# Optimization experiments

Measured on AMD Instinct MI355X. Metric: run time of the kernel, lower is better.

## Reference

```python
import jax, jax.numpy as jnp
import numpy as np

H = 2048
EPS = 1e-5  # torch LayerNorm default

def layer_norm(x, g, b):
    mu = jnp.mean(x, axis=-1, keepdims=True)
    var = jnp.mean(jnp.square(x - mu), axis=-1, keepdims=True)
    return (x - mu) * jax.lax.rsqrt(var + EPS) * g + b

def setup_inputs() -> dict:
    key = jax.random.key(0)
    ks = jax.random.split(key, 5)
    bound = 1.0 / np.sqrt(H)  # torch Linear default init range
    x = jax.random.normal(ks[0], (8192, H), dtype=jnp.float32)
    W1 = jax.random.uniform(ks[1], (H, H), jnp.float32, -bound, bound)
    b1 = jax.random.uniform(ks[2], (H,), jnp.float32, -bound, bound)
    W2 = jax.random.uniform(ks[3], (H, H), jnp.float32, -bound, bound)
    b2 = jax.random.uniform(ks[4], (H,), jnp.float32, -bound, bound)
    g1 = jnp.ones((H,), jnp.float32); be1 = jnp.zeros((H,), jnp.float32)
    g2 = jnp.ones((H,), jnp.float32); be2 = jnp.zeros((H,), jnp.float32)
    return {"x": x, "W1": W1, "b1": b1, "W2": W2, "b2": b2,
            "g1": g1, "be1": be1, "g2": g2, "be2": be2}

def reference(x, W1, b1, W2, b2, g1, be1, g2, be2):
    # ln1 -> linear1 -> relu -> (dropout p=0) -> ln2 -> linear2 -> (dropout p=0) -> +x -> relu
    out = layer_norm(x, g1, be1)
    out = jax.nn.relu(out @ W1.T + b1)
    out = layer_norm(out, g2, be2)
    out = out @ W2.T + b2
    return jax.nn.relu(out + x)
```

## Files before the change

### kernel.cpp

```cpp
#include <hip/hip_runtime.h>
#include <hip/hip_bf16.h>

#define H_DIM 2048
#define LN_EPS 1e-5f

typedef __bf16 bf16_t;
typedef __bf16 bf16x4 __attribute__((ext_vector_type(4)));
typedef __bf16 bf16x8 __attribute__((ext_vector_type(8)));
typedef float f32x4 __attribute__((ext_vector_type(4)));

__device__ __forceinline__ void async_copy16(const void* g, void* l) {
    __builtin_amdgcn_global_load_lds((const __attribute__((address_space(1))) void*)g,
                                     (__attribute__((address_space(3))) void*)l,
                                     16, 0, 0);
}

#define FENCE() asm volatile("" ::: "memory")
#define BARRIER() do { FENCE(); __builtin_amdgcn_s_barrier(); FENCE(); } while (0)

__global__ __launch_bounds__(256) void cast2_kernel(const float* __restrict__ w1,
                                                    const float* __restrict__ w2,
                                                    bf16_t* __restrict__ o1,
                                                    bf16_t* __restrict__ o2) {
    const int n4 = (H_DIM * H_DIM) / 4;
    int i = blockIdx.x * 256 + threadIdx.x;
    const float* src; bf16_t* dst; int j;
    if (i < n4) { src = w1; dst = o1; j = i; }
    else        { src = w2; dst = o2; j = i - n4; }
    float4 v = reinterpret_cast<const float4*>(src)[j];
    bf16x4 r;
    r[0] = (bf16_t)v.x; r[1] = (bf16_t)v.y; r[2] = (bf16_t)v.z; r[3] = (bf16_t)v.w;
    reinterpret_cast<bf16x4*>(dst)[j] = r;
}

__global__ __launch_bounds__(256) void ln_f32_v2(const float* __restrict__ in,
                                                 const float* __restrict__ g,
                                                 const float* __restrict__ b,
                                                 bf16_t* __restrict__ out,
                                                 bf16_t* __restrict__ xb) {
    const int l = threadIdx.x & 63, w = threadIdx.x >> 6;
    const size_t row = (size_t)blockIdx.x * 4 + w;
    const float* xr = in + row * H_DIM;
    float4 v[8];
    #pragma unroll
    for (int k = 0; k < 8; ++k) v[k] = reinterpret_cast<const float4*>(xr)[l + k * 64];
    float s = 0.f, s2 = 0.f;
    #pragma unroll
    for (int k = 0; k < 8; ++k) {
        s  += v[k].x + v[k].y + v[k].z + v[k].w;
        s2 += v[k].x * v[k].x + v[k].y * v[k].y + v[k].z * v[k].z + v[k].w * v[k].w;
    }
    #pragma unroll
    for (int off = 32; off > 0; off >>= 1) {
        s  += __shfl_down(s,  off, 64);
        s2 += __shfl_down(s2, off, 64);
    }
    s  = __shfl(s,  0, 64);
    s2 = __shfl(s2, 0, 64);
    float mu   = s * (1.f / H_DIM);
    float rstd = rsqrtf(s2 * (1.f / H_DIM) - mu * mu + LN_EPS);
    bf16_t* orow = out + row * H_DIM;
    bf16_t* xrow = xb ? xb + row * H_DIM : nullptr;
    #pragma unroll
    for (int k = 0; k < 8; ++k) {
        int c = l + k * 64;
        float4 gv = reinterpret_cast<const float4*>(g)[c];
        float4 bv = reinterpret_cast<const float4*>(b)[c];
        bf16x4 y;
        y[0] = (bf16_t)((v[k].x - mu) * rstd * gv.x + bv.x);
        y[1] = (bf16_t)((v[k].y - mu) * rstd * gv.y + bv.y);
        y[2] = (bf16_t)((v[k].z - mu) * rstd * gv.z + bv.z);
        y[3] = (bf16_t)((v[k].w - mu) * rstd * gv.w + bv.w);
        reinterpret_cast<bf16x4*>(orow)[c] = y;
        if (xrow) {
            bf16x4 xv;
            xv[0] = (bf16_t)v[k].x; xv[1] = (bf16_t)v[k].y;
            xv[2] = (bf16_t)v[k].z; xv[3] = (bf16_t)v[k].w;
            reinterpret_cast<bf16x4*>(xrow)[c] = xv;
        }
    }
}

__global__ __launch_bounds__(256) void ln_bf16_v2(const bf16_t* __restrict__ in,
                                                  const float* __restrict__ g,
                                                  const float* __restrict__ b,
                                                  bf16_t* __restrict__ out) {
    const int l = threadIdx.x & 63, w = threadIdx.x >> 6;
    const size_t row = (size_t)blockIdx.x * 4 + w;
    const bf16_t* xr = in + row * H_DIM;
    bf16x8 xv[4];
    #pragma unroll
    for (int k = 0; k < 4; ++k) xv[k] = reinterpret_cast<const bf16x8*>(xr)[l + k * 64];
    float vv[32];
    #pragma unroll
    for (int k = 0; k < 4; ++k)
        #pragma unroll
        for (int j = 0; j < 8; ++j) vv[k * 8 + j] = (float)xv[k][j];
    float s = 0.f, s2 = 0.f;
    #pragma unroll
    for (int e = 0; e < 32; ++e) { s += vv[e]; s2 += vv[e] * vv[e]; }
    #pragma unroll
    for (int off = 32; off > 0; off >>= 1) {
        s  += __shfl_down(s,  off, 64);
        s2 += __shfl_down(s2, off, 64);
    }
    s  = __shfl(s,  0, 64);
    s2 = __shfl(s2, 0, 64);
    float mu   = s * (1.f / H_DIM);
    float rstd = rsqrtf(s2 * (1.f / H_DIM) - mu * mu + LN_EPS);
    bf16_t* orow = out + row * H_DIM;
    #pragma unroll
    for (int k = 0; k < 4; ++k) {
        int c = l + k * 64;
        float4 g0 = reinterpret_cast<const float4*>(g)[c * 2];
        float4 g1 = reinterpret_cast<const float4*>(g)[c * 2 + 1];
        float4 b0 = reinterpret_cast<const float4*>(b)[c * 2];
        float4 b1 = reinterpret_cast<const float4*>(b)[c * 2 + 1];
        bf16x8 y;
        y[0] = (bf16_t)((vv[k*8+0] - mu) * rstd * g0.x + b0.x);
        y[1] = (bf16_t)((vv[k*8+1] - mu) * rstd * g0.y + b0.y);
        y[2] = (bf16_t)((vv[k*8+2] - mu) * rstd * g0.z + b0.z);
        y[3] = (bf16_t)((vv[k*8+3] - mu) * rstd * g0.w + b0.w);
        y[4] = (bf16_t)((vv[k*8+4] - mu) * rstd * g1.x + b1.x);
        y[5] = (bf16_t)((vv[k*8+5] - mu) * rstd * g1.y + b1.y);
        y[6] = (bf16_t)((vv[k*8+6] - mu) * rstd * g1.z + b1.z);
        y[7] = (bf16_t)((vv[k*8+7] - mu) * rstd * g1.w + b1.w);
        reinterpret_cast<bf16x8*>(orow)[c] = y;
    }
}

#define LDW 88

template<int FINAL, int RB>
__global__ __launch_bounds__(512, 2) void gemm8_kernel(
    const bf16_t* __restrict__ A,
    const bf16_t* __restrict__ B,
    const float*  __restrict__ bias,
    const float*  __restrict__ residf,
    const bf16_t* __restrict__ residb,
    bf16_t* __restrict__ obf,
    float*  __restrict__ of)
{
    __shared__ bf16_t sm[8 * 8192];

    const int tid = threadIdx.x;
    const int l  = tid & 63, w = tid >> 6;
    const int wm = w >> 2,  wn = w & 3;
    const int cl = l & 15,  ch = l >> 4;

    const int cpx = gridDim.x >> 3;
    const int bid = blockIdx.x;
    const int swz = (bid & 7) * cpx + (bid >> 3);
    const size_t row0 = (size_t)(swz >> 3) * 256;
    const size_t col0 = (size_t)(swz & 7) * 256;

    const bf16_t* Abase = A + row0 * H_DIM;
    const bf16_t* Bbase = B + col0 * H_DIM;

    const int rr  = w * 8 + (l >> 3);
    const int scb = (l & 7) ^ (l >> 3);
    const size_t soff  = (size_t)rr * H_DIM + scb * 8;
    const int ldsw0 = w * 512;
    const int ldsw1 = 4096 + w * 512;

    const int swx = cl & 7;
    const int cbks[2] = { ch ^ swx, (4 + ch) ^ swx };

    f32x4 acc[2][4][4] = {};

    auto STAGE = [&](const bf16_t* Gb, int kt, int half, int region) {
        const bf16_t* g = Gb + (size_t)half * (128 * H_DIM) + kt * 64 + soff;
        bf16_t* s = &sm[region * 8192];
        async_copy16(g,               s + ldsw0);
        async_copy16(g + 64 * H_DIM,  s + ldsw1);
    };
    auto RDA = [&](int buf, int mh, int m, int ks) -> bf16x8 {
        int r = mh * 64 + m * 16 + cl;
        return *(const bf16x8*)&sm[(buf * 4 + wm) * 8192 + r * 64 + cbks[ks] * 8];
    };
    auto RDB = [&](int buf, int n, int ks) -> bf16x8 {
        int r = (wn & 1) * 64 + n * 16 + cl;
        return *(const bf16x8*)&sm[(buf * 4 + 2 + (wn >> 1)) * 8192 + r * 64 + cbks[ks] * 8];
    };

    auto KT = [&](int buf, int t, bool stA, bool stB, int vm) {
        bf16x8 a[4], b0[4], b1[4];
        #pragma unroll
        for (int n = 0; n < 4; ++n) b0[n] = RDB(buf, n, 0);
        #pragma unroll
        for (int m = 0; m < 4; ++m) a[m] = RDA(buf, 0, m, 0);
        if (stA) STAGE(Abase, t + 1, 0, (buf ^ 1) * 4 + 0);
        BARRIER();
        __builtin_amdgcn_s_setprio(1);
        #pragma unroll
        for (int m = 0; m < 4; ++m)
            #pragma unroll
            for (int n = 0; n < 4; ++n)
                acc[0][m][n] = __builtin_amdgcn_mfma_f32_16x16x32_bf16(a[m], b0[n], acc[0][m][n], 0, 0, 0);
        __builtin_amdgcn_s_setprio(0);
        BARRIER();
        #pragma unroll
        for (int n = 0; n < 4; ++n) b1[n] = RDB(buf, n, 1);
        #pragma unroll
        for (int m = 0; m < 4; ++m) a[m] = RDA(buf, 0, m, 1);
        if (stA) STAGE(Abase, t + 1, 1, (buf ^ 1) * 4 + 1);
        BARRIER();
        __builtin_amdgcn_s_setprio(1);
        #pragma unroll
        for (int m = 0; m < 4; ++m)
            #pragma unroll
            for (int n = 0; n < 4; ++n)
                acc[0][m][n] = __builtin_amdgcn_mfma_f32_16x16x32_bf16(a[m], b1[n], acc[0][m][n], 0, 0, 0);
        __builtin_amdgcn_s_setprio(0);
        BARRIER();
        #pragma unroll
        for (int m = 0; m < 4; ++m) a[m] = RDA(buf, 1, m, 0);
        if (stB) STAGE(Bbase, t + 2, 0, buf * 4 + 2);
        BARRIER();
        __builtin_amdgcn_s_setprio(1);
        #pragma unroll
        for (int m = 0; m < 4; ++m)
            #pragma unroll
            for (int n = 0; n < 4; ++n)
                acc[1][m][n] = __builtin_amdgcn_mfma_f32_16x16x32_bf16(a[m], b0[n], acc[1][m][n], 0, 0, 0);
        __builtin_amdgcn_s_setprio(0);
        BARRIER();
        #pragma unroll
        for (int m = 0; m < 4; ++m) a[m] = RDA(buf, 1, m, 1);
        if (stB) STAGE(Bbase, t + 2, 1, buf * 4 + 3);
        BARRIER();
        __builtin_amdgcn_s_setprio(1);
        #pragma unroll
        for (int m = 0; m < 4; ++m)
            #pragma unroll
            for (int n = 0; n < 4; ++n)
                acc[1][m][n] = __builtin_amdgcn_mfma_f32_16x16x32_bf16(a[m], b1[n], acc[1][m][n], 0, 0, 0);
        __builtin_amdgcn_s_setprio(0);
        if (vm == 4)      asm volatile("s_waitcnt vmcnt(4)");
        else if (vm == 0) asm volatile("s_waitcnt vmcnt(0)");
        BARRIER();
    };

    STAGE(Abase, 0, 0, 0); STAGE(Abase, 0, 1, 1);
    STAGE(Bbase, 0, 0, 2); STAGE(Bbase, 0, 1, 3);
    STAGE(Bbase, 1, 0, 6); STAGE(Bbase, 1, 1, 7);
    asm volatile("s_waitcnt vmcnt(4)");
    BARRIER();

    for (int t = 0; t < 30; t += 2) {
        KT(0, t,     true, true, 4);
        KT(1, t + 1, true, true, 4);
    }
    KT(0, 30, true,  false, 0);
    KT(1, 31, false, false, -1);

    if constexpr (FINAL) {
        #pragma unroll
        for (int mh = 0; mh < 2; ++mh)
            #pragma unroll
            for (int m = 0; m < 4; ++m)
                #pragma unroll
                for (int n = 0; n < 4; ++n) {
                    size_t col = col0 + wn * 64 + n * 16 + cl;
                    float bv = bias[col];
                    #pragma unroll
                    for (int j = 0; j < 4; ++j) {
                        size_t row = row0 + wm * 128 + mh * 64 + m * 16 + ch * 4 + j;
                        size_t idx = row * H_DIM + col;
                        float rv = RB ? (float)residb[idx] : residf[idx];
                        of[idx] = fmaxf(acc[mh][m][n][j] + bv + rv, 0.f);
                    }
                }
    } else {
        bf16_t* wls = (bf16_t*)((char*)sm + w * (64 * LDW * 2));
        #pragma unroll
        for (int mh = 0; mh < 2; ++mh) {
            #pragma unroll
            for (int m = 0; m < 4; ++m)
                #pragma unroll
                for (int n = 0; n < 4; ++n) {
                    float bv = bias[col0 + wn * 64 + n * 16 + cl];
                    #pragma unroll
                    for (int j = 0; j < 4; ++j) {
                        int lr = m * 16 + ch * 4 + j;
                        int lc = n * 16 + cl;
                        wls[lr * LDW + lc] = (bf16_t)fmaxf(acc[mh][m][n][j] + bv, 0.f);
                    }
                }
            #pragma unroll
            for (int k = 0; k < 8; ++k) {
                int c = l + k * 64;
                int r = c >> 3, cb = c & 7;
                bf16x8 vv = *(const bf16x8*)&wls[r * LDW + cb * 8];
                size_t grow = row0 + wm * 128 + mh * 64 + r;
                *(bf16x8*)&obf[grow * H_DIM + col0 + wn * 64 + cb * 8] = vv;
            }
        }
    }
}

extern "C" void kernel_launch(void* const* d_in, const int* in_sizes, int n_in,
                              void* d_out, int out_size, void* d_ws, size_t ws_size,
                              hipStream_t stream) {
    const float* x   = (const float*)d_in[0];
    const float* W1  = (const float*)d_in[1];
    const float* b1  = (const float*)d_in[2];
    const float* W2  = (const float*)d_in[3];
    const float* b2  = (const float*)d_in[4];
    const float* g1  = (const float*)d_in[5];
    const float* be1 = (const float*)d_in[6];
    const float* g2  = (const float*)d_in[7];
    const float* be2 = (const float*)d_in[8];
    float* out = (float*)d_out;

    const int M = in_sizes[0] / H_DIM;

    char* ws = (char*)d_ws;
    bf16_t* W1b = (bf16_t*)(ws);
    bf16_t* W2b = (bf16_t*)(ws + (8u << 20));
    bf16_t* lnb = (bf16_t*)(ws + (16u << 20));
    bf16_t* h1  = (bf16_t*)(ws + (48u << 20));
    const bool use_xb = ws_size >= ((size_t)96 << 20);
    bf16_t* xb  = use_xb ? (bf16_t*)(ws + (80u << 20)) : nullptr;

    const int n4tot = 2 * (H_DIM * H_DIM) / 4;
    cast2_kernel<<<dim3(n4tot / 256), dim3(256), 0, stream>>>(W1, W2, W1b, W2b);

    ln_f32_v2<<<dim3(M / 4), dim3(256), 0, stream>>>(x, g1, be1, lnb, xb);

    gemm8_kernel<0, 0><<<dim3((M / 256) * 8), dim3(512), 0, stream>>>(
        lnb, W1b, b1, nullptr, nullptr, h1, nullptr);

    ln_bf16_v2<<<dim3(M / 4), dim3(256), 0, stream>>>(h1, g2, be2, lnb);

    if (use_xb) {
        gemm8_kernel<1, 1><<<dim3((M / 256) * 8), dim3(512), 0, stream>>>(
            lnb, W2b, b2, nullptr, xb, nullptr, out);
    } else {
        gemm8_kernel<1, 0><<<dim3((M / 256) * 8), dim3(512), 0, stream>>>(
            lnb, W2b, b2, x, nullptr, nullptr, out);
    }
}
```

Measured before the change: 302.7 us.

## Merge weight cast with LN1, halve GEMM barriers, stage residual through LDS

Merges the weight-cast kernel and the first LayerNorm into one launch, so one kernel launch and its tail idle time go away. In the GEMM inner step, both k-slices of A and B fragments are now loaded up front and two MFMA batches run per barrier phase, cutting the barriers per K-tile from eight to four. The cost is higher register pressure, which could cause spills under launch_bounds(512,2). Bias loads are hoisted out of the epilogues. In the final bf16-residual path, residual tiles are first loaded coalesced into LDS and then read per fragment, replacing the strided global reads.

```diff
diff --git a/kernel.cpp b/kernel.cpp
--- a/kernel.cpp
+++ b/kernel.cpp
@@ -18,29 +18,31 @@
 #define FENCE() asm volatile("" ::: "memory")
 #define BARRIER() do { FENCE(); __builtin_amdgcn_s_barrier(); FENCE(); } while (0)
 
-__global__ __launch_bounds__(256) void cast2_kernel(const float* __restrict__ w1,
-                                                    const float* __restrict__ w2,
-                                                    bf16_t* __restrict__ o1,
-                                                    bf16_t* __restrict__ o2) {
-    const int n4 = (H_DIM * H_DIM) / 4;
-    int i = blockIdx.x * 256 + threadIdx.x;
-    const float* src; bf16_t* dst; int j;
-    if (i < n4) { src = w1; dst = o1; j = i; }
-    else        { src = w2; dst = o2; j = i - n4; }
-    float4 v = reinterpret_cast<const float4*>(src)[j];
-    bf16x4 r;
-    r[0] = (bf16_t)v.x; r[1] = (bf16_t)v.y; r[2] = (bf16_t)v.z; r[3] = (bf16_t)v.w;
-    reinterpret_cast<bf16x4*>(dst)[j] = r;
-}
-
-__global__ __launch_bounds__(256) void ln_f32_v2(const float* __restrict__ in,
-                                                 const float* __restrict__ g,
-                                                 const float* __restrict__ b,
-                                                 bf16_t* __restrict__ out,
-                                                 bf16_t* __restrict__ xb) {
-    const int l = threadIdx.x & 63, w = threadIdx.x >> 6;
-    const size_t row = (size_t)blockIdx.x * 4 + w;
-    const float* xr = in + row * H_DIM;
+__global__ __launch_bounds__(256) void pre_kernel(const float* __restrict__ w1,
+                                                  const float* __restrict__ w2,
+                                                  bf16_t* __restrict__ o1,
+                                                  bf16_t* __restrict__ o2,
+                                                  const float* __restrict__ x,
+                                                  const float* __restrict__ g,
+                                                  const float* __restrict__ b,
+                                                  bf16_t* __restrict__ lnb,
+                                                  bf16_t* __restrict__ xb) {
+    const int bid = blockIdx.x, t = threadIdx.x;
+    if (bid < 8192) {
+        const int n4 = (H_DIM * H_DIM) / 4;
+        int i = bid * 256 + t;
+        const float* src; bf16_t* dst; int j;
+        if (i < n4) { src = w1; dst = o1; j = i; }
+        else        { src = w2; dst = o2; j = i - n4; }
+        float4 v = reinterpret_cast<const float4*>(src)[j];
+        bf16x4 r;
+        r[0] = (bf16_t)v.x; r[1] = (bf16_t)v.y; r[2] = (bf16_t)v.z; r[3] = (bf16_t)v.w;
+        reinterpret_cast<bf16x4*>(dst)[j] = r;
+        return;
+    }
+    const int l = t & 63, w = t >> 6;
+    const size_t row = (size_t)(bid - 8192) * 4 + w;
+    const float* xr = x + row * H_DIM;
     float4 v[8];
     #pragma unroll
     for (int k = 0; k < 8; ++k) v[k] = reinterpret_cast<const float4*>(xr)[l + k * 64];
@@ -59,7 +61,7 @@
     s2 = __shfl(s2, 0, 64);
     float mu   = s * (1.f / H_DIM);
     float rstd = rsqrtf(s2 * (1.f / H_DIM) - mu * mu + LN_EPS);
-    bf16_t* orow = out + row * H_DIM;
+    bf16_t* orow = lnb + row * H_DIM;
     bf16_t* xrow = xb ? xb + row * H_DIM : nullptr;
     #pragma unroll
     for (int k = 0; k < 8; ++k) {
@@ -130,6 +132,7 @@
 }
 
 #define LDW 88
+#define RPW 264
 
 template<int FINAL, int RB>
 __global__ __launch_bounds__(512, 2) void gemm8_kernel(
@@ -165,6 +168,10 @@
 
     const int swx = cl & 7;
     const int cbks[2] = { ch ^ swx, (4 + ch) ^ swx };
+
+    float bv[4];
+    #pragma unroll
+    for (int n = 0; n < 4; ++n) bv[n] = bias[col0 + wn * 64 + n * 16 + cl];
 
     f32x4 acc[2][4][4] = {};
 
@@ -184,57 +191,43 @@
     };
 
     auto KT = [&](int buf, int t, bool stA, bool stB, int vm) {
-        bf16x8 a[4], b0[4], b1[4];
-        #pragma unroll
-        for (int n = 0; n < 4; ++n) b0[n] = RDB(buf, n, 0);
-        #pragma unroll
-        for (int m = 0; m < 4; ++m) a[m] = RDA(buf, 0, m, 0);
-        if (stA) STAGE(Abase, t + 1, 0, (buf ^ 1) * 4 + 0);
+        bf16x8 a0[4], a1[4], b0[4], b1[4];
+        #pragma unroll
+        for (int n = 0; n < 4; ++n) { b0[n] = RDB(buf, n, 0); b1[n] = RDB(buf, n, 1); }
+        #pragma unroll
+        for (int m = 0; m < 4; ++m) { a0[m] = RDA(buf, 0, m, 0); a1[m] = RDA(buf, 0, m, 1); }
+        if (stA) { STAGE(Abase, t + 1, 0, (buf ^ 1) * 4 + 0);
+                   STAGE(Abase, t + 1, 1, (buf ^ 1) * 4 + 1); }
         BARRIER();
         __builtin_amdgcn_s_setprio(1);
         #pragma unroll
         for (int m = 0; m < 4; ++m)
             #pragma unroll
             for (int n = 0; n < 4; ++n)
-                acc[0][m][n] = __builtin_amdgcn_mfma_f32_16x16x32_bf16(a[m], b0[n], acc[0][m][n], 0, 0, 0);
+                acc[0][m][n] = __builtin_amdgcn_mfma_f32_16x16x32_bf16(a0[m], b0[n], acc[0][m][n], 0, 0, 0);
+        #pragma unroll
+        for (int m = 0; m < 4; ++m)
+            #pragma unroll
+            for (int n = 0; n < 4; ++n)
+                acc[0][m][n] = __builtin_amdgcn_mfma_f32_16x16x32_bf16(a1[m], b1[n], acc[0][m][n], 0, 0, 0);
         __builtin_amdgcn_s_setprio(0);
         BARRIER();
         #pragma unroll
-        for (int n = 0; n < 4; ++n) b1[n] = RDB(buf, n, 1);
-        #pragma unroll
-        for (int m = 0; m < 4; ++m) a[m] = RDA(buf, 0, m, 1);
-        if (stA) STAGE(Abase, t + 1, 1, (buf ^ 1) * 4 + 1);
+        for (int m = 0; m < 4; ++m) { a0[m] = RDA(buf, 1, m, 0); a1[m] = RDA(buf, 1, m, 1); }
+        if (stB) { STAGE(Bbase, t + 2, 0, buf * 4 + 2);
+                   STAGE(Bbase, t + 2, 1, buf * 4 + 3); }
         BARRIER();
         __builtin_amdgcn_s_setprio(1);
         #pragma unroll
         for (int m = 0; m < 4; ++m)
             #pragma unroll
             for (int n = 0; n < 4; ++n)
-                acc[0][m][n] = __builtin_amdgcn_mfma_f32_16x16x32_bf16(a[m], b1[n], acc[0][m][n], 0, 0, 0);
-        __builtin_amdgcn_s_setprio(0);
-        BARRIER();
-        #pragma unroll
-        for (int m = 0; m < 4; ++m) a[m] = RDA(buf, 1, m, 0);
-        if (stB) STAGE(Bbase, t + 2, 0, buf * 4 + 2);
-        BARRIER();
-        __builtin_amdgcn_s_setprio(1);
+                acc[1][m][n] = __builtin_amdgcn_mfma_f32_16x16x32_bf16(a0[m], b0[n], acc[1][m][n], 0, 0, 0);
         #pragma unroll
         for (int m = 0; m < 4; ++m)
             #pragma unroll
             for (int n = 0; n < 4; ++n)
-                acc[1][m][n] = __builtin_amdgcn_mfma_f32_16x16x32_bf16(a[m], b0[n], acc[1][m][n], 0, 0, 0);
-        __builtin_amdgcn_s_setprio(0);
-        BARRIER();
-        #pragma unroll
-        for (int m = 0; m < 4; ++m) a[m] = RDA(buf, 1, m, 1);
-        if (stB) STAGE(Bbase, t + 2, 1, buf * 4 + 3);
-        BARRIER();
-        __builtin_amdgcn_s_setprio(1);
-        #pragma unroll
-        for (int m = 0; m < 4; ++m)
-            #pragma unroll
-            for (int n = 0; n < 4; ++n)
-                acc[1][m][n] = __builtin_amdgcn_mfma_f32_16x16x32_bf16(a[m], b1[n], acc[1][m][n], 0, 0, 0);
+                acc[1][m][n] = __builtin_amdgcn_mfma_f32_16x16x32_bf16(a1[m], b1[n], acc[1][m][n], 0, 0, 0);
         __builtin_amdgcn_s_setprio(0);
         if (vm == 4)      asm volatile("s_waitcnt vmcnt(4)");
         else if (vm == 0) asm volatile("s_waitcnt vmcnt(0)");
@@ -255,38 +248,63 @@
     KT(1, 31, false, false, -1);
 
     if constexpr (FINAL) {
-        #pragma unroll
-        for (int mh = 0; mh < 2; ++mh)
+        if constexpr (RB) {
+            #pragma unroll
+            for (int p = 0; p < 2; ++p) {
+                #pragma unroll
+                for (int i = 0; i < 8; ++i) {
+                    int c = i * 512 + tid;
+                    int u = c >> 5, cb = c & 31;
+                    size_t gr = row0 + (size_t)(u >> 6) * 128 + p * 64 + (u & 63);
+                    bf16x8 vv = *(const bf16x8*)&residb[gr * H_DIM + col0 + cb * 8];
+                    *(bf16x8*)&sm[u * RPW + cb * 8] = vv;
+                }
+                BARRIER();
+                #pragma unroll
+                for (int m = 0; m < 4; ++m)
+                    #pragma unroll
+                    for (int n = 0; n < 4; ++n) {
+                        size_t col = col0 + wn * 64 + n * 16 + cl;
+                        #pragma unroll
+                        for (int j = 0; j < 4; ++j) {
+                            int u = wm * 64 + m * 16 + ch * 4 + j;
+                            size_t row = row0 + wm * 128 + p * 64 + m * 16 + ch * 4 + j;
+                            float rv = (float)sm[u * RPW + wn * 64 + n * 16 + cl];
+                            of[row * H_DIM + col] = fmaxf(acc[p][m][n][j] + bv[n] + rv, 0.f);
+                        }
+                    }
+                BARRIER();
+            }
+        } else {
+            #pragma unroll
+            for (int mh = 0; mh < 2; ++mh)
+                #pragma unroll
+                for (int m = 0; m < 4; ++m)
+                    #pragma unroll
+                    for (int n = 0; n < 4; ++n) {
+                        size_t col = col0 + wn * 64 + n * 16 + cl;
+                        #pragma unroll
+                        for (int j = 0; j < 4; ++j) {
+                            size_t row = row0 + wm * 128 + mh * 64 + m * 16 + ch * 4 + j;
+                            size_t idx = row * H_DIM + col;
+                            of[idx] = fmaxf(acc[mh][m][n][j] + bv[n] + residf[idx], 0.f);
+                        }
+                    }
+        }
+    } else {
+        bf16_t* wls = (bf16_t*)((char*)sm + w * (64 * LDW * 2));
+        #pragma unroll
+        for (int mh = 0; mh < 2; ++mh) {
             #pragma unroll
             for (int m = 0; m < 4; ++m)
                 #pragma unroll
-                for (int n = 0; n < 4; ++n) {
-                    size_t col = col0 + wn * 64 + n * 16 + cl;
-                    float bv = bias[col];
-                    #pragma unroll
-                    for (int j = 0; j < 4; ++j) {
-                        size_t row = row0 + wm * 128 + mh * 64 + m * 16 + ch * 4 + j;
-                        size_t idx = row * H_DIM + col;
-                        float rv = RB ? (float)residb[idx] : residf[idx];
-                        of[idx] = fmaxf(acc[mh][m][n][j] + bv + rv, 0.f);
-                    }
-                }
-    } else {
-        bf16_t* wls = (bf16_t*)((char*)sm + w * (64 * LDW * 2));
-        #pragma unroll
-        for (int mh = 0; mh < 2; ++mh) {
-            #pragma unroll
-            for (int m = 0; m < 4; ++m)
-                #pragma unroll
-                for (int n = 0; n < 4; ++n) {
-                    float bv = bias[col0 + wn * 64 + n * 16 + cl];
+                for (int n = 0; n < 4; ++n)
                     #pragma unroll
                     for (int j = 0; j < 4; ++j) {
                         int lr = m * 16 + ch * 4 + j;
                         int lc = n * 16 + cl;
-                        wls[lr * LDW + lc] = (bf16_t)fmaxf(acc[mh][m][n][j] + bv, 0.f);
+                        wls[lr * LDW + lc] = (bf16_t)fmaxf(acc[mh][m][n][j] + bv[n], 0.f);
                     }
-                }
             #pragma unroll
             for (int k = 0; k < 8; ++k) {
                 int c = l + k * 64;
@@ -323,10 +341,8 @@
     const bool use_xb = ws_size >= ((size_t)96 << 20);
     bf16_t* xb  = use_xb ? (bf16_t*)(ws + (80u << 20)) : nullptr;
 
-    const int n4tot = 2 * (H_DIM * H_DIM) / 4;
-    cast2_kernel<<<dim3(n4tot / 256), dim3(256), 0, stream>>>(W1, W2, W1b, W2b);
-
-    ln_f32_v2<<<dim3(M / 4), dim3(256), 0, stream>>>(x, g1, be1, lnb, xb);
+    pre_kernel<<<dim3(8192 + M / 4), dim3(256), 0, stream>>>(
+        W1, W2, W1b, W2b, x, g1, be1, lnb, xb);
 
     gemm8_kernel<0, 0><<<dim3((M / 256) * 8), dim3(512), 0, stream>>>(
         lnb, W1b, b1, nullptr, nullptr, h1, nullptr);
```

Measured after the change: 297.0 us. No clear change (-1.9%).
